# Kernel tuning notes

Hardware: AMD Instinct MI355X
Metric: run time of the kernel (lower is better)

The kernel has to match this reference:

```python
import jax, jax.numpy as jnp
import numpy as np

B, S, D, H, F = 4, 2048, 256, 8, 2  # batch, seq, input_size, heads, mlp factor
EPS = 1e-5


def _ln(x, g, b):
    m = jnp.mean(x, axis=-1, keepdims=True)
    v = jnp.var(x, axis=-1, keepdims=True)
    return (x - m) / jnp.sqrt(v + EPS) * g + b


def setup_inputs() -> dict:
    key = jax.random.key(0)
    ks = jax.random.split(key, 12)
    s = 1.0 / np.sqrt(D)
    return {
        "X":  jax.random.normal(ks[0], (B, S, D), jnp.float32),
        # Wide attention: each of H heads has full [D,D] Q/K/V projections (no bias)
        "Wq": jax.random.uniform(ks[1], (H, D, D), jnp.float32, -s, s),
        "Wk": jax.random.uniform(ks[2], (H, D, D), jnp.float32, -s, s),
        "Wv": jax.random.uniform(ks[3], (H, D, D), jnp.float32, -s, s),
        "Wz": jax.random.uniform(ks[4], (H * D, D), jnp.float32, -1.0 / np.sqrt(H * D), 1.0 / np.sqrt(H * D)),
        "bz": jnp.zeros((D,), jnp.float32),
        "W1": jax.random.uniform(ks[5], (D, F * D), jnp.float32, -s, s),
        "b1": jnp.zeros((F * D,), jnp.float32),
        "W2": jax.random.uniform(ks[6], (F * D, D), jnp.float32, -1.0 / np.sqrt(F * D), 1.0 / np.sqrt(F * D)),
        "b2": jnp.zeros((D,), jnp.float32),
        "g1": jnp.ones((D,), jnp.float32),
        "be1": jnp.zeros((D,), jnp.float32),
        "g2": jnp.ones((D,), jnp.float32),
        "be2": jnp.zeros((D,), jnp.float32),
    }


def reference(X, Wq, Wk, Wv, Wz, bz, W1, b1, W2, b2, g1, be1, g2, be2):
    scale = D ** (-0.25)  # applied to both q and k as in the source
    q = jnp.einsum('bsd,hde->hbse', X, Wq) * scale   # [H,B,S,D]
    k = jnp.einsum('btd,hde->hbte', X, Wk) * scale
    v = jnp.einsum('btd,hde->hbte', X, Wv)
    attn = jax.nn.softmax(jnp.einsum('hbse,hbte->hbst', q, k), axis=-1)  # [H,B,S,S]
    zh = jnp.einsum('hbst,hbte->hbse', attn, v)       # [H,B,S,D]
    # concat heads along feature dim (head order matters for Wz)
    zcat = jnp.transpose(zh, (1, 2, 0, 3)).reshape(B, S, H * D)
    z = zcat @ Wz + bz
    z = _ln(z + X, g1, be1)                            # dropout p=0 -> identity
    z_ff = jnp.maximum(z @ W1 + b1, 0.0) @ W2 + b2
    z = _ln(z_ff + z, g2, be2)
    attn_mean = jnp.mean(attn, axis=0)                 # [B,S,S]
    return z, attn_mean
```

## Files before the change

### kernel.cpp

```cpp
#include <hip/hip_runtime.h>
#include <cstdint>
#include <cstddef>

#define B_  4
#define S_  2048
#define D_  256
#define H_  8
#define FD_ 512
#define N_  (B_*S_)
#define HD_ (H_*D_)
#define EPS 1e-5f

typedef __attribute__((ext_vector_type(8))) short bf16x8;
typedef __attribute__((ext_vector_type(8))) unsigned short u16x8;
typedef __attribute__((ext_vector_type(4))) float f32x4;

__device__ __forceinline__ unsigned short f2bf(float f) {
  union { float f; unsigned u; } x; x.f = f;
  unsigned u = x.u;
  return (unsigned short)((u + 0x7FFFu + ((u >> 16) & 1u)) >> 16);
}
__device__ __forceinline__ float bf2f(unsigned short h) {
  union { unsigned u; float f; } x; x.u = ((unsigned)h) << 16; return x.f;
}

__device__ __forceinline__ void glds16(const void* gptr, void* ldsptr) {
  __builtin_amdgcn_global_load_lds(
      (__attribute__((address_space(1))) void*)gptr,
      (__attribute__((address_space(3))) void*)ldsptr,
      16, 0, 0);
}

__device__ __forceinline__ int sw32(int row, int u) {
  return (row*32 + ((u & 24) | ((u & 7) ^ (row & 7)))) * 8;
}
__device__ __forceinline__ int sw16(int row, int u) {
  return (row*16 + ((u & 8) | ((u & 7) ^ (row & 7)))) * 8;
}

__global__ __launch_bounds__(256) void cast_x_kernel(
    const float* __restrict__ X, unsigned short* __restrict__ Xb)
{
  const size_t i8 = ((size_t)blockIdx.x * 256 + threadIdx.x) * 8;
  float4 a = *(const float4*)&X[i8];
  float4 b = *(const float4*)&X[i8 + 4];
  u16x8 o;
  o[0]=f2bf(a.x); o[1]=f2bf(a.y); o[2]=f2bf(a.z); o[3]=f2bf(a.w);
  o[4]=f2bf(b.x); o[5]=f2bf(b.y); o[6]=f2bf(b.z); o[7]=f2bf(b.w);
  *(u16x8*)&Xb[i8] = o;
}

__global__ __launch_bounds__(256) void prep_w_kernel(
    const float* __restrict__ Wq, const float* __restrict__ Wk,
    const float* __restrict__ Wv, unsigned short* __restrict__ Wt)
{
  __shared__ float tile[64][65];
  const int tid = threadIdx.x;
  const int d0 = blockIdx.x * 64, e0 = blockIdx.y * 64;
  const int w = blockIdx.z;
  const float* src;
  float scale;
  if (w < 8)       { src = Wq + (size_t)w*D_*D_;      scale = 0.25f; }
  else if (w < 16) { src = Wk + (size_t)(w-8)*D_*D_;  scale = 0.25f; }
  else             { src = Wv + (size_t)(w-16)*D_*D_; scale = 1.0f;  }
  {
    int r = tid >> 2, c16 = (tid & 3) * 16;
    const float* s = src + (size_t)(d0 + r)*D_ + e0 + c16;
    #pragma unroll
    for (int u = 0; u < 4; ++u) *(float4*)&tile[r][c16 + u*4] = *(const float4*)(s + u*4);
  }
  __syncthreads();
  {
    int er = tid >> 2, dc = (tid & 3) * 16;
    u16x8 o0, o1;
    #pragma unroll
    for (int j = 0; j < 8; ++j) {
      o0[j] = f2bf(tile[dc + j][er] * scale);
      o1[j] = f2bf(tile[dc + 8 + j][er] * scale);
    }
    unsigned short* dst = Wt + ((size_t)w*D_ + e0 + er)*D_ + d0 + dc;
    *(u16x8*)(dst)     = o0;
    *(u16x8*)(dst + 8) = o1;
  }
}

__global__ __launch_bounds__(256) void tcast_kernel(
    const float* __restrict__ src, unsigned short* __restrict__ dst,
    int R, int C)
{
  __shared__ float tile[64][65];
  const int tid = threadIdx.x;
  const int r0 = blockIdx.x * 64, c0 = blockIdx.y * 64;
  {
    int r = tid >> 2, c16 = (tid & 3) * 16;
    const float* s = src + (size_t)(r0 + r)*C + c0 + c16;
    #pragma unroll
    for (int u = 0; u < 4; ++u) *(float4*)&tile[r][c16 + u*4] = *(const float4*)(s + u*4);
  }
  __syncthreads();
  {
    int cr = tid >> 2, rc = (tid & 3) * 16;
    u16x8 o0, o1;
    #pragma unroll
    for (int j = 0; j < 8; ++j) {
      o0[j] = f2bf(tile[rc + j][cr]);
      o1[j] = f2bf(tile[rc + 8 + j][cr]);
    }
    unsigned short* d = dst + (size_t)(c0 + cr)*R + r0 + rc;
    *(u16x8*)(d)     = o0;
    *(u16x8*)(d + 8) = o1;
  }
}

__global__ __launch_bounds__(256) void qkv_kernel(
    const unsigned short* __restrict__ Xb, const unsigned short* __restrict__ Wt,
    unsigned short* __restrict__ q, unsigned short* __restrict__ k,
    unsigned short* __restrict__ v)
{
  __shared__ unsigned short Xt[64*32*8];
  __shared__ unsigned short Wtile[64*32*8];
  const int tid = threadIdx.x;
  const int w4 = tid >> 6, lane = tid & 63;
  const int c = lane & 15, qd = lane >> 4;
  const int n0 = blockIdx.x * 64;
  const int e0 = blockIdx.y * 64;
  const int w  = blockIdx.z;

  unsigned short* obase;
  if (w < 8)       obase = q + (size_t)w*N_*D_;
  else if (w < 16) obase = k + (size_t)(w-8)*N_*D_;
  else             obase = v + (size_t)(w-16)*N_*D_;

  {
    const char* xg = (const char*)Xb + (size_t)n0*512;
    const char* wg = (const char*)Wt + ((size_t)w*D_ + e0)*512;
    #pragma unroll
    for (int i = 0; i < 8; ++i) {
      int g = w4*8 + i;
      int r = 2*g + (lane >> 5);
      int su = lane & 31;
      int u = (su & 24) | ((su & 7) ^ (r & 7));
      glds16(xg + (size_t)r*512 + u*16, &Xt[g*512]);
      glds16(wg + (size_t)r*512 + u*16, &Wtile[g*512]);
    }
  }
  __syncthreads();

  f32x4 sc[4];
  #pragma unroll
  for (int nc = 0; nc < 4; ++nc) sc[nc] = (f32x4){0.f,0.f,0.f,0.f};
  #pragma unroll
  for (int ks = 0; ks < 8; ++ks) {
    bf16x8 xa = *(const bf16x8*)&Xt[sw32(16*w4 + c, ks*4 + qd)];
    #pragma unroll
    for (int nc = 0; nc < 4; ++nc) {
      bf16x8 bf = *(const bf16x8*)&Wtile[sw32(nc*16 + c, ks*4 + qd)];
      sc[nc] = __builtin_amdgcn_mfma_f32_16x16x32_bf16(xa, bf, sc[nc], 0, 0, 0);
    }
  }
  #pragma unroll
  for (int nc = 0; nc < 4; ++nc)
    #pragma unroll
    for (int r = 0; r < 4; ++r)
      obase[(size_t)(n0 + 16*w4 + qd*4 + r)*D_ + e0 + nc*16 + c] = f2bf(sc[nc][r]);
}

__global__ __launch_bounds__(256) void vtrans_kernel(
    const unsigned short* __restrict__ vb, unsigned short* __restrict__ vT)
{
  __shared__ unsigned short tile[64][72];
  const int tid = threadIdx.x;
  const int t0 = blockIdx.x * 64, e0 = blockIdx.y * 64;
  const int h = blockIdx.z >> 2, b = blockIdx.z & 3;
  const size_t in_base = (size_t)h*N_*D_ + (size_t)b*S_*D_;
  {
    int r = tid >> 2, c16 = (tid & 3) * 16;
    const unsigned short* src = vb + in_base + (size_t)(t0 + r)*D_ + e0 + c16;
    *(u16x8*)&tile[r][c16]     = *(const u16x8*)(src);
    *(u16x8*)&tile[r][c16 + 8] = *(const u16x8*)(src + 8);
  }
  __syncthreads();
  {
    int er = tid >> 2, tt = (tid & 3) * 16;
    u16x8 o0, o1;
    #pragma unroll
    for (int j = 0; j < 8; ++j) { o0[j] = tile[tt+j][er]; o1[j] = tile[tt+8+j][er]; }
    unsigned short* dst = vT + ((size_t)(h*4 + b)*D_ + e0 + er)*S_ + t0 + tt;
    *(u16x8*)(dst)     = o0;
    *(u16x8*)(dst + 8) = o1;
  }
}

__global__ __launch_bounds__(256, 2) void attn_ol_kernel(
    const unsigned short* __restrict__ qb, const unsigned short* __restrict__ kb,
    const unsigned short* __restrict__ vT, unsigned short* __restrict__ zcatb,
    float* __restrict__ Lws)
{
  __shared__ unsigned short Kt[2][32*32*8];
  __shared__ unsigned short Vt[2][16*544];
  const int tid = threadIdx.x;
  const int w = tid >> 6, lane = tid & 63;
  const int c = lane & 15, qd = lane >> 4;
  const int wg = blockIdx.x;
  const int xcd = wg & 7;
  const int slot = wg >> 3;
  const int j = slot & 15;
  const int gg = slot >> 4;
  const int g = gg*8 + xcd;
  const int h = g >> 2, b = g & 3;
  const int s0 = j * 128;

  const size_t qkbase = (size_t)h*N_*D_ + (size_t)b*S_*D_;

  bf16x8 qa[2][8];
  #pragma unroll
  for (int mi = 0; mi < 2; ++mi) {
    const unsigned short* qrow = qb + qkbase + (size_t)(s0 + 32*w + 16*mi + c)*D_ + qd*8;
    #pragma unroll
    for (int ks = 0; ks < 8; ++ks) qa[mi][ks] = *(const bf16x8*)(qrow + ks*32);
  }

  f32x4 o[2][16];
  #pragma unroll
  for (int mi = 0; mi < 2; ++mi)
    #pragma unroll
    for (int i = 0; i < 16; ++i) o[mi][i] = (f32x4){0.f,0.f,0.f,0.f};
  float Lp[2] = {0.f, 0.f};

  const char* kB = (const char*)(kb + qkbase);
  const char* vB = (const char*)(vT + (size_t)(h*4 + b)*D_*S_);

  #define STAGE_OL(kt_, bi_)                                                   \
    {                                                                          \
      _Pragma("unroll")                                                        \
      for (int i = 0; i < 4; ++i) {                                            \
        int gq = w*4 + i;                                                      \
        int r = 2*gq + (lane >> 5);                                            \
        int Lg = ((r >> 2) & 3)*8 + (r >> 4)*4 + (r & 3);                      \
        int su = lane & 31;                                                    \
        int u = (su & 24) | ((su & 7) ^ (r & 7));                              \
        glds16(kB + ((size_t)(kt_)*32 + Lg)*512 + u*16, &Kt[bi_][gq*512]);     \
      }                                                                        \
      _Pragma("unroll")                                                        \
      for (int i = 0; i < 4; ++i) {                                            \
        int gq = w*4 + i;                                                      \
        int e = gq*16 + (lane >> 2);                                           \
        int qv = (lane & 3) ^ ((lane >> 3) & 3);                               \
        glds16(vB + (size_t)e*4096 + (size_t)(kt_)*64 + qv*16, &Vt[bi_][gq*544]);\
      }                                                                        \
    }

  STAGE_OL(0, 0);

  for (int kt = 0; kt < 64; ++kt) {
    const int bi = kt & 1;
    __syncthreads();
    if (kt + 1 < 64) STAGE_OL(kt + 1, bi ^ 1);

    f32x4 sc[2][2];
    #pragma unroll
    for (int mi = 0; mi < 2; ++mi)
      #pragma unroll
      for (int nc = 0; nc < 2; ++nc) sc[mi][nc] = (f32x4){0.f,0.f,0.f,0.f};
    #pragma unroll
    for (int ks = 0; ks < 8; ++ks) {
      bf16x8 kf0 = *(const bf16x8*)&Kt[bi][sw32(c,      ks*4 + qd)];
      bf16x8 kf1 = *(const bf16x8*)&Kt[bi][sw32(16 + c, ks*4 + qd)];
      #pragma unroll
      for (int mi = 0; mi < 2; ++mi) {
        sc[mi][0] = __builtin_amdgcn_mfma_f32_16x16x32_bf16(kf0, qa[mi][ks], sc[mi][0], 0, 0, 0);
        sc[mi][1] = __builtin_amdgcn_mfma_f32_16x16x32_bf16(kf1, qa[mi][ks], sc[mi][1], 0, 0, 0);
      }
    }
    bf16x8 pa[2];
    #pragma unroll
    for (int mi = 0; mi < 2; ++mi) {
      float ex[2][4];
      #pragma unroll
      for (int nc = 0; nc < 2; ++nc)
        #pragma unroll
        for (int r = 0; r < 4; ++r) {
          float p = __expf(sc[mi][nc][r]);
          ex[nc][r] = p;
          Lp[mi] += p;
        }
      union { unsigned u[4]; bf16x8 v; } cv;
      asm("v_cvt_pk_bf16_f32 %0, %1, %2" : "=v"(cv.u[0]) : "v"(ex[0][0]), "v"(ex[0][1]));
      asm("v_cvt_pk_bf16_f32 %0, %1, %2" : "=v"(cv.u[1]) : "v"(ex[0][2]), "v"(ex[0][3]));
      asm("v_cvt_pk_bf16_f32 %0, %1, %2" : "=v"(cv.u[2]) : "v"(ex[1][0]), "v"(ex[1][1]));
      asm("v_cvt_pk_bf16_f32 %0, %1, %2" : "=v"(cv.u[3]) : "v"(ex[1][2]), "v"(ex[1][3]));
      pa[mi] = cv.v;
    }
    #pragma unroll
    for (int ec = 0; ec < 16; ++ec) {
      bf16x8 vf = *(const bf16x8*)&Vt[bi][ec*544 + c*32 + (qd ^ ((c >> 1) & 3))*8];
      o[0][ec] = __builtin_amdgcn_mfma_f32_16x16x32_bf16(pa[0], vf, o[0][ec], 0, 0, 0);
      o[1][ec] = __builtin_amdgcn_mfma_f32_16x16x32_bf16(pa[1], vf, o[1][ec], 0, 0, 0);
    }
  }

  #pragma unroll
  for (int mi = 0; mi < 2; ++mi) {
    float L = Lp[mi];
    L += __shfl_xor(L, 16);
    L += __shfl_xor(L, 32);
    if (qd == 0)
      Lws[(size_t)h*N_ + b*S_ + s0 + 32*w + 16*mi + c] = L;
    float il[4];
    #pragma unroll
    for (int r = 0; r < 4; ++r)
      il[r] = 1.0f / __shfl(L, (lane & 48) | (qd*4 + r));
    #pragma unroll
    for (int ec = 0; ec < 16; ++ec)
      #pragma unroll
      for (int r = 0; r < 4; ++r)
        zcatb[(size_t)(b*S_ + s0 + 32*w + 16*mi + qd*4 + r)*HD_ + h*D_ + ec*16 + c] =
            f2bf(o[mi][ec][r] * il[r]);
  }
  #undef STAGE_OL
}

#define FATSMEM (73728 + 512)
__global__ __launch_bounds__(256, 2) void attn_mean_wz_kernel(
    const unsigned short* __restrict__ qb, const unsigned short* __restrict__ kb,
    const float* __restrict__ Lws, float* __restrict__ out_attn,
    const unsigned short* __restrict__ zcatb, const unsigned short* __restrict__ Wzt,
    const float* __restrict__ bz, const float* __restrict__ X,
    const float* __restrict__ g1, const float* __restrict__ be1,
    unsigned short* __restrict__ z1b)
{
  __shared__ __align__(16) char smem[FATSMEM];
  const int tid = threadIdx.x;
  const int w = tid >> 6, lane = tid & 63;
  const int c = lane & 15, qd = lane >> 4;
  const int bid = blockIdx.x;

  if (bid < 2048) {
    unsigned short (*Kt)[64*32*8] = (unsigned short (*)[64*32*8])smem;
    const int xcd = bid & 7;
    const int slot = bid >> 3;
    const int j = slot & 15;
    const int ggg = slot >> 4;
    const int g = ggg*8 + xcd;
    const int b = g >> 5;
    const int t0 = (g & 31) * 64;
    const int s0 = j * 128;

    float am[2][4][4] = {};

    #define STAGE_AM(h_, bi_)                                                  \
      {                                                                        \
        const char* kB = (const char*)(kb + (size_t)(h_)*N_*D_ + (size_t)b*S_*D_);\
        _Pragma("unroll")                                                      \
        for (int i = 0; i < 8; ++i) {                                          \
          int gq = w*8 + i;                                                    \
          int r = 2*gq + (lane >> 5);                                          \
          int su = lane & 31;                                                  \
          int u = (su & 24) | ((su & 7) ^ (r & 7));                            \
          glds16(kB + ((size_t)t0 + r)*512 + u*16, &Kt[bi_][gq*512]);          \
        }                                                                      \
      }

    STAGE_AM(0, 0);

    bf16x8 qa[2][8];
    #pragma unroll
    for (int mi = 0; mi < 2; ++mi) {
      const unsigned short* qrow = qb + (size_t)b*S_*D_ + (size_t)(s0 + 32*w + 16*mi + c)*D_ + qd*8;
      #pragma unroll
      for (int ks = 0; ks < 8; ++ks) qa[mi][ks] = *(const bf16x8*)(qrow + ks*32);
    }

    for (int h = 0; h < 8; ++h) {
      const int bi = h & 1;
      __syncthreads();
      if (h + 1 < 8) STAGE_AM(h + 1, bi ^ 1);

      float il[2][4];
      #pragma unroll
      for (int mi = 0; mi < 2; ++mi)
        #pragma unroll
        for (int r = 0; r < 4; ++r)
          il[mi][r] = 0.125f / Lws[(size_t)h*N_ + b*S_ + s0 + 32*w + 16*mi + qd*4 + r];

      bf16x8 qn[2][8];
      if (h + 1 < 8) {
        const size_t basen = (size_t)(h+1)*N_*D_ + (size_t)b*S_*D_;
        #pragma unroll
        for (int mi = 0; mi < 2; ++mi) {
          const unsigned short* qrow = qb + basen + (size_t)(s0 + 32*w + 16*mi + c)*D_ + qd*8;
          #pragma unroll
          for (int ks = 0; ks < 8; ++ks) qn[mi][ks] = *(const bf16x8*)(qrow + ks*32);
        }
      }

      f32x4 sc[2][4];
      #pragma unroll
      for (int mi = 0; mi < 2; ++mi)
        #pragma unroll
        for (int nc = 0; nc < 4; ++nc) sc[mi][nc] = (f32x4){0.f,0.f,0.f,0.f};
      #pragma unroll
      for (int ks = 0; ks < 8; ++ks) {
        #pragma unroll
        for (int nc = 0; nc < 4; ++nc) {
          bf16x8 kf = *(const bf16x8*)&Kt[bi][sw32(nc*16 + c, ks*4 + qd)];
          sc[0][nc] = __builtin_amdgcn_mfma_f32_16x16x32_bf16(qa[0][ks], kf, sc[0][nc], 0, 0, 0);
          sc[1][nc] = __builtin_amdgcn_mfma_f32_16x16x32_bf16(qa[1][ks], kf, sc[1][nc], 0, 0, 0);
        }
      }
      #pragma unroll
      for (int mi = 0; mi < 2; ++mi)
        #pragma unroll
        for (int nc = 0; nc < 4; ++nc)
          #pragma unroll
          for (int r = 0; r < 4; ++r)
            am[mi][nc][r] += __expf(sc[mi][nc][r]) * il[mi][r];

      if (h + 1 < 8) {
        #pragma unroll
        for (int mi = 0; mi < 2; ++mi)
          #pragma unroll
          for (int ks = 0; ks < 8; ++ks) qa[mi][ks] = qn[mi][ks];
      }
    }
    #pragma unroll
    for (int mi = 0; mi < 2; ++mi)
      #pragma unroll
      for (int nc = 0; nc < 4; ++nc)
        #pragma unroll
        for (int r = 0; r < 4; ++r)
          out_attn[(size_t)(b*S_ + s0 + 32*w + 16*mi + qd*4 + r)*S_ + t0 + nc*16 + c] =
              am[mi][nc][r];
    #undef STAGE_AM
  } else {
    unsigned short* At  = (unsigned short*)smem;
    unsigned short* Wt2 = (unsigned short*)(smem + 8192);
    float (*redS)[32] = (float (*)[32])(smem + 73728);
    float (*redQ)[32] = (float (*)[32])(smem + 73728 + 256);
    const int n0 = (bid - 2048) * 32;
    const int w4 = w;
    const int msub = w4 & 1, ehalf = w4 >> 1;

    f32x4 acc[8];
    #pragma unroll
    for (int nc = 0; nc < 8; ++nc) acc[nc] = (f32x4){0.f,0.f,0.f,0.f};

    for (int kc = 0; kc < 16; ++kc) {
      {
        const char* ab = (const char*)zcatb + (size_t)n0*4096 + (size_t)kc*256;
        #pragma unroll
        for (int i = 0; i < 2; ++i) {
          int g = w4*2 + i;
          int r = g*4 + (lane >> 4);
          int su = lane & 15;
          int u = (su & 8) | ((su & 7) ^ (r & 7));
          glds16(ab + (size_t)r*4096 + u*16, &At[g*512]);
        }
        const char* wb = (const char*)Wzt + (size_t)kc*256;
        #pragma unroll
        for (int i = 0; i < 16; ++i) {
          int g = w4*16 + i;
          int e = g*4 + (lane >> 4);
          int su = lane & 15;
          int u = (su & 8) | ((su & 7) ^ (e & 7));
          glds16(wb + (size_t)e*4096 + u*16, &Wt2[g*512]);
        }
      }
      __syncthreads();
      #pragma unroll
      for (int ks = 0; ks < 4; ++ks) {
        bf16x8 a = *(const bf16x8*)&At[sw16(msub*16 + c, ks*4 + qd)];
        #pragma unroll
        for (int nc = 0; nc < 8; ++nc) {
          bf16x8 bv = *(const bf16x8*)&Wt2[sw16(ehalf*128 + nc*16 + c, ks*4 + qd)];
          acc[nc] = __builtin_amdgcn_mfma_f32_16x16x32_bf16(a, bv, acc[nc], 0, 0, 0);
        }
      }
      __syncthreads();
    }

    float vals[8][4];
    float sum_[4] = {0.f,0.f,0.f,0.f}, sq_[4] = {0.f,0.f,0.f,0.f};
    #pragma unroll
    for (int nc = 0; nc < 8; ++nc) {
      int e = ehalf*128 + nc*16 + c;
      #pragma unroll
      for (int r = 0; r < 4; ++r) {
        int n = n0 + msub*16 + qd*4 + r;
        float v = acc[nc][r] + bz[e] + X[(size_t)n*D_ + e];
        vals[nc][r] = v;
        sum_[r] += v; sq_[r] += v*v;
      }
    }
    #pragma unroll
    for (int off = 1; off < 16; off <<= 1) {
      #pragma unroll
      for (int r = 0; r < 4; ++r) {
        sum_[r] += __shfl_xor(sum_[r], off);
        sq_[r]  += __shfl_xor(sq_[r],  off);
      }
    }
    if (c == 0) {
      #pragma unroll
      for (int r = 0; r < 4; ++r) {
        redS[ehalf][msub*16 + qd*4 + r] = sum_[r];
        redQ[ehalf][msub*16 + qd*4 + r] = sq_[r];
      }
    }
    __syncthreads();
    #pragma unroll
    for (int r = 0; r < 4; ++r) {
      int lr = msub*16 + qd*4 + r;
      float Sv = redS[0][lr] + redS[1][lr];
      float Qv = redQ[0][lr] + redQ[1][lr];
      float mean = Sv * (1.0f/D_);
      float var  = Qv * (1.0f/D_) - mean*mean;
      float rstd = rsqrtf(var + EPS);
      int n = n0 + lr;
      #pragma unroll
      for (int nc = 0; nc < 8; ++nc) {
        int e = ehalf*128 + nc*16 + c;
        z1b[(size_t)n*D_ + e] = f2bf((vals[nc][r] - mean)*rstd*g1[e] + be1[e]);
      }
    }
  }
}

__global__ __launch_bounds__(256) void mlp1_kernel(
    const unsigned short* __restrict__ z1b, const unsigned short* __restrict__ W1t,
    const float* __restrict__ b1, unsigned short* __restrict__ hbuf)
{
  __shared__ unsigned short At[64*32*8];
  __shared__ unsigned short Bt[64*32*8];
  const int tid = threadIdx.x;
  const int w4 = tid >> 6, lane = tid & 63;
  const int c = lane & 15, qd = lane >> 4;
  const int n0 = blockIdx.x * 64;
  const int f0 = blockIdx.y * 64;

  {
    const char* ag = (const char*)z1b + (size_t)n0*512;
    const char* bg = (const char*)W1t + (size_t)f0*512;
    #pragma unroll
    for (int i = 0; i < 8; ++i) {
      int g = w4*8 + i;
      int r = 2*g + (lane >> 5);
      int su = lane & 31;
      int u = (su & 24) | ((su & 7) ^ (r & 7));
      glds16(ag + (size_t)r*512 + u*16, &At[g*512]);
      glds16(bg + (size_t)r*512 + u*16, &Bt[g*512]);
    }
  }
  __syncthreads();

  f32x4 sc[4];
  #pragma unroll
  for (int nc = 0; nc < 4; ++nc) sc[nc] = (f32x4){0.f,0.f,0.f,0.f};
  #pragma unroll
  for (int ks = 0; ks < 8; ++ks) {
    bf16x8 xa = *(const bf16x8*)&At[sw32(16*w4 + c, ks*4 + qd)];
    #pragma unroll
    for (int nc = 0; nc < 4; ++nc) {
      bf16x8 bf = *(const bf16x8*)&Bt[sw32(nc*16 + c, ks*4 + qd)];
      sc[nc] = __builtin_amdgcn_mfma_f32_16x16x32_bf16(xa, bf, sc[nc], 0, 0, 0);
    }
  }
  #pragma unroll
  for (int nc = 0; nc < 4; ++nc) {
    int f = f0 + nc*16 + c;
    float bias = b1[f];
    #pragma unroll
    for (int r = 0; r < 4; ++r)
      hbuf[(size_t)(n0 + 16*w4 + qd*4 + r)*FD_ + f] = f2bf(fmaxf(sc[nc][r] + bias, 0.f));
  }
}

__global__ __launch_bounds__(256) void mlp2_kernel(
    const unsigned short* __restrict__ hbuf, const unsigned short* __restrict__ W2t,
    const float* __restrict__ b2, const unsigned short* __restrict__ z1b,
    const float* __restrict__ g2, const float* __restrict__ be2,
    float* __restrict__ out)
{
  __shared__ unsigned short At[32*16*8];
  __shared__ unsigned short Wt2[256*16*8];
  __shared__ float redS[2][32], redQ[2][32];
  const int tid = threadIdx.x;
  const int w4 = tid >> 6, lane = tid & 63;
  const int c = lane & 15, qd = lane >> 4;
  const int n0 = blockIdx.x * 32;
  const int msub = w4 & 1, ehalf = w4 >> 1;

  f32x4 acc[8];
  #pragma unroll
  for (int nc = 0; nc < 8; ++nc) acc[nc] = (f32x4){0.f,0.f,0.f,0.f};

  for (int kc = 0; kc < 4; ++kc) {
    {
      const char* ab = (const char*)hbuf + (size_t)n0*1024 + (size_t)kc*256;
      #pragma unroll
      for (int i = 0; i < 2; ++i) {
        int g = w4*2 + i;
        int r = g*4 + (lane >> 4);
        int su = lane & 15;
        int u = (su & 8) | ((su & 7) ^ (r & 7));
        glds16(ab + (size_t)r*1024 + u*16, &At[g*512]);
      }
      const char* wb = (const char*)W2t + (size_t)kc*256;
      #pragma unroll
      for (int i = 0; i < 16; ++i) {
        int g = w4*16 + i;
        int e = g*4 + (lane >> 4);
        int su = lane & 15;
        int u = (su & 8) | ((su & 7) ^ (e & 7));
        glds16(wb + (size_t)e*1024 + u*16, &Wt2[g*512]);
      }
    }
    __syncthreads();
    #pragma unroll
    for (int ks = 0; ks < 4; ++ks) {
      bf16x8 a = *(const bf16x8*)&At[sw16(msub*16 + c, ks*4 + qd)];
      #pragma unroll
      for (int nc = 0; nc < 8; ++nc) {
        bf16x8 bv = *(const bf16x8*)&Wt2[sw16(ehalf*128 + nc*16 + c, ks*4 + qd)];
        acc[nc] = __builtin_amdgcn_mfma_f32_16x16x32_bf16(a, bv, acc[nc], 0, 0, 0);
      }
    }
    __syncthreads();
  }

  float vals[8][4];
  float sum_[4] = {0.f,0.f,0.f,0.f}, sq_[4] = {0.f,0.f,0.f,0.f};
  #pragma unroll
  for (int nc = 0; nc < 8; ++nc) {
    int e = ehalf*128 + nc*16 + c;
    #pragma unroll
    for (int r = 0; r < 4; ++r) {
      int n = n0 + msub*16 + qd*4 + r;
      float v = acc[nc][r] + b2[e] + bf2f(z1b[(size_t)n*D_ + e]);
      vals[nc][r] = v;
      sum_[r] += v; sq_[r] += v*v;
    }
  }
  #pragma unroll
  for (int off = 1; off < 16; off <<= 1) {
    #pragma unroll
    for (int r = 0; r < 4; ++r) {
      sum_[r] += __shfl_xor(sum_[r], off);
      sq_[r]  += __shfl_xor(sq_[r],  off);
    }
  }
  if (c == 0) {
    #pragma unroll
    for (int r = 0; r < 4; ++r) {
      redS[ehalf][msub*16 + qd*4 + r] = sum_[r];
      redQ[ehalf][msub*16 + qd*4 + r] = sq_[r];
    }
  }
  __syncthreads();
  #pragma unroll
  for (int r = 0; r < 4; ++r) {
    int lr = msub*16 + qd*4 + r;
    float Sv = redS[0][lr] + redS[1][lr];
    float Qv = redQ[0][lr] + redQ[1][lr];
    float mean = Sv * (1.0f/D_);
    float var  = Qv * (1.0f/D_) - mean*mean;
    float rstd = rsqrtf(var + EPS);
    int n = n0 + lr;
    #pragma unroll
    for (int nc = 0; nc < 8; ++nc) {
      int e = ehalf*128 + nc*16 + c;
      out[(size_t)n*D_ + e] = (vals[nc][r] - mean)*rstd*g2[e] + be2[e];
    }
  }
}

extern "C" void kernel_launch(void* const* d_in, const int* in_sizes, int n_in,
                              void* d_out, int out_size, void* d_ws, size_t ws_size,
                              hipStream_t stream)
{
  (void)in_sizes; (void)n_in; (void)out_size; (void)ws_size;
  const float* X   = (const float*)d_in[0];
  const float* Wq  = (const float*)d_in[1];
  const float* Wk  = (const float*)d_in[2];
  const float* Wv  = (const float*)d_in[3];
  const float* Wz  = (const float*)d_in[4];
  const float* bz  = (const float*)d_in[5];
  const float* W1  = (const float*)d_in[6];
  const float* b1  = (const float*)d_in[7];
  const float* W2  = (const float*)d_in[8];
  const float* b2  = (const float*)d_in[9];
  const float* g1  = (const float*)d_in[10];
  const float* be1 = (const float*)d_in[11];
  const float* g2  = (const float*)d_in[12];
  const float* be2 = (const float*)d_in[13];

  char* p = (char*)d_ws;
  unsigned short* Xbb  = (unsigned short*)p; p += (size_t)N_*D_*2;
  unsigned short* Wtb  = (unsigned short*)p; p += (size_t)24*D_*D_*2;
  unsigned short* Wztb = (unsigned short*)p; p += (size_t)D_*HD_*2;
  unsigned short* W1tb = (unsigned short*)p; p += (size_t)FD_*D_*2;
  unsigned short* W2tb = (unsigned short*)p; p += (size_t)D_*FD_*2;
  unsigned short* qbuf = (unsigned short*)p; p += (size_t)H_*N_*D_*2;
  unsigned short* kbuf = (unsigned short*)p; p += (size_t)H_*N_*D_*2;
  unsigned short* vbuf = (unsigned short*)p; p += (size_t)H_*N_*D_*2;
  unsigned short* vTb  = (unsigned short*)p; p += (size_t)H_*N_*D_*2;
  float* Lws   = (float*)p; p += (size_t)H_*N_*4;
  unsigned short* zcatb = (unsigned short*)p; p += (size_t)N_*HD_*2;
  unsigned short* z1b   = (unsigned short*)p; p += (size_t)N_*D_*2;
  unsigned short* hbuf  = (unsigned short*)p;

  float* out_z    = (float*)d_out;
  float* out_attn = out_z + (size_t)N_*D_;

  cast_x_kernel<<<N_*D_/(256*8), 256, 0, stream>>>(X, Xbb);

  dim3 gW(4, 4, 24);
  prep_w_kernel<<<gW, 256, 0, stream>>>(Wq, Wk, Wv, Wtb);

  { dim3 g(HD_/64, D_/64);  tcast_kernel<<<g, 256, 0, stream>>>(Wz, Wztb, HD_, D_); }
  { dim3 g(D_/64, FD_/64);  tcast_kernel<<<g, 256, 0, stream>>>(W1, W1tb, D_, FD_); }
  { dim3 g(FD_/64, D_/64);  tcast_kernel<<<g, 256, 0, stream>>>(W2, W2tb, FD_, D_); }

  dim3 gA(N_/64, D_/64, 24);
  qkv_kernel<<<gA, 256, 0, stream>>>(Xbb, Wtb, qbuf, kbuf, vbuf);

  dim3 gT(S_/64, D_/64, H_*B_);
  vtrans_kernel<<<gT, 256, 0, stream>>>(vbuf, vTb);

  attn_ol_kernel<<<512, 256, 0, stream>>>(qbuf, kbuf, vTb, zcatb, Lws);

  attn_mean_wz_kernel<<<2304, 256, 0, stream>>>(
      qbuf, kbuf, Lws, out_attn, zcatb, Wztb, bz, X, g1, be1, z1b);

  dim3 gM1(N_/64, FD_/64);
  mlp1_kernel<<<gM1, 256, 0, stream>>>(z1b, W1tb, b1, hbuf);

  mlp2_kernel<<<N_/32, 256, 0, stream>>>(hbuf, W2tb, b2, z1b, g2, be2, out_z);
}
```

Measured before the change: 527.0 us.

## Merge prep kernels into one launch and fuse V transpose into QKV GEMM

Five preprocessing launches (X cast, QKV weight transpose/scale, and the Wz/W1/W2 transposes) become a single kernel that picks its task from the block index. The QKV projection kernel now writes V already transposed, staging the tile through the reused X shared buffer, so the separate vtrans kernel and the round trip of V through global memory are gone. This saves launch overhead and about 32 MB of memory traffic, at the cost of two extra barriers in the V-producing blocks and branchier prep code.

```diff
diff --git a/kernel.cpp b/kernel.cpp
--- a/kernel.cpp
+++ b/kernel.cpp
@@ -38,62 +38,68 @@
   return (row*16 + ((u & 8) | ((u & 7) ^ (row & 7)))) * 8;
 }
 
-__global__ __launch_bounds__(256) void cast_x_kernel(
-    const float* __restrict__ X, unsigned short* __restrict__ Xb)
-{
-  const size_t i8 = ((size_t)blockIdx.x * 256 + threadIdx.x) * 8;
-  float4 a = *(const float4*)&X[i8];
-  float4 b = *(const float4*)&X[i8 + 4];
-  u16x8 o;
-  o[0]=f2bf(a.x); o[1]=f2bf(a.y); o[2]=f2bf(a.z); o[3]=f2bf(a.w);
-  o[4]=f2bf(b.x); o[5]=f2bf(b.y); o[6]=f2bf(b.z); o[7]=f2bf(b.w);
-  *(u16x8*)&Xb[i8] = o;
-}
-
-__global__ __launch_bounds__(256) void prep_w_kernel(
+__global__ __launch_bounds__(256) void prep_fat_kernel(
+    const float* __restrict__ X, unsigned short* __restrict__ Xb,
     const float* __restrict__ Wq, const float* __restrict__ Wk,
-    const float* __restrict__ Wv, unsigned short* __restrict__ Wt)
+    const float* __restrict__ Wv, unsigned short* __restrict__ Wt,
+    const float* __restrict__ Wz, unsigned short* __restrict__ Wzt,
+    const float* __restrict__ W1, unsigned short* __restrict__ W1t,
+    const float* __restrict__ W2, unsigned short* __restrict__ W2t)
 {
   __shared__ float tile[64][65];
   const int tid = threadIdx.x;
-  const int d0 = blockIdx.x * 64, e0 = blockIdx.y * 64;
-  const int w = blockIdx.z;
+  const int bid = blockIdx.x;
+
+  if (bid < 1024) {
+    const size_t i8 = ((size_t)bid * 256 + tid) * 8;
+    float4 a = *(const float4*)&X[i8];
+    float4 b = *(const float4*)&X[i8 + 4];
+    u16x8 o;
+    o[0]=f2bf(a.x); o[1]=f2bf(a.y); o[2]=f2bf(a.z); o[3]=f2bf(a.w);
+    o[4]=f2bf(b.x); o[5]=f2bf(b.y); o[6]=f2bf(b.z); o[7]=f2bf(b.w);
+    *(u16x8*)&Xb[i8] = o;
+    return;
+  }
+
   const float* src;
-  float scale;
-  if (w < 8)       { src = Wq + (size_t)w*D_*D_;      scale = 0.25f; }
-  else if (w < 16) { src = Wk + (size_t)(w-8)*D_*D_;  scale = 0.25f; }
-  else             { src = Wv + (size_t)(w-16)*D_*D_; scale = 1.0f;  }
+  unsigned short* dst_base;
+  int R, C;
+  float scale = 1.0f;
+  int d0, e0;
+  bool is_prepw = false;
+  int wsel = 0;
+
+  if (bid < 1408) {
+    int idx = bid - 1024;
+    d0 = (idx & 3) * 64;
+    e0 = ((idx >> 2) & 3) * 64;
+    wsel = idx >> 4;
+    if (wsel < 8)       { src = Wq + (size_t)wsel*D_*D_;      scale = 0.25f; }
+    else if (wsel < 16) { src = Wk + (size_t)(wsel-8)*D_*D_;  scale = 0.25f; }
+    else                { src = Wv + (size_t)(wsel-16)*D_*D_; scale = 1.0f;  }
+    R = D_; C = D_;
+    dst_base = Wt;
+    is_prepw = true;
+  } else if (bid < 1536) {
+    int idx = bid - 1408;
+    d0 = (idx & 31) * 64;
+    e0 = (idx >> 5) * 64;
+    src = Wz; dst_base = Wzt; R = HD_; C = D_;
+  } else if (bid < 1568) {
+    int idx = bid - 1536;
+    d0 = (idx & 3) * 64;
+    e0 = (idx >> 2) * 64;
+    src = W1; dst_base = W1t; R = D_; C = FD_;
+  } else {
+    int idx = bid - 1568;
+    d0 = (idx & 7) * 64;
+    e0 = (idx >> 3) * 64;
+    src = W2; dst_base = W2t; R = FD_; C = D_;
+  }
+
   {
     int r = tid >> 2, c16 = (tid & 3) * 16;
-    const float* s = src + (size_t)(d0 + r)*D_ + e0 + c16;
-    #pragma unroll
-    for (int u = 0; u < 4; ++u) *(float4*)&tile[r][c16 + u*4] = *(const float4*)(s + u*4);
-  }
-  __syncthreads();
-  {
-    int er = tid >> 2, dc = (tid & 3) * 16;
-    u16x8 o0, o1;
-    #pragma unroll
-    for (int j = 0; j < 8; ++j) {
-      o0[j] = f2bf(tile[dc + j][er] * scale);
-      o1[j] = f2bf(tile[dc + 8 + j][er] * scale);
-    }
-    unsigned short* dst = Wt + ((size_t)w*D_ + e0 + er)*D_ + d0 + dc;
-    *(u16x8*)(dst)     = o0;
-    *(u16x8*)(dst + 8) = o1;
-  }
-}
-
-__global__ __launch_bounds__(256) void tcast_kernel(
-    const float* __restrict__ src, unsigned short* __restrict__ dst,
-    int R, int C)
-{
-  __shared__ float tile[64][65];
-  const int tid = threadIdx.x;
-  const int r0 = blockIdx.x * 64, c0 = blockIdx.y * 64;
-  {
-    int r = tid >> 2, c16 = (tid & 3) * 16;
-    const float* s = src + (size_t)(r0 + r)*C + c0 + c16;
+    const float* s = src + (size_t)(d0 + r)*C + e0 + c16;
     #pragma unroll
     for (int u = 0; u < 4; ++u) *(float4*)&tile[r][c16 + u*4] = *(const float4*)(s + u*4);
   }
@@ -103,10 +109,14 @@
     u16x8 o0, o1;
     #pragma unroll
     for (int j = 0; j < 8; ++j) {
-      o0[j] = f2bf(tile[rc + j][cr]);
-      o1[j] = f2bf(tile[rc + 8 + j][cr]);
-    }
-    unsigned short* d = dst + (size_t)(c0 + cr)*R + r0 + rc;
+      o0[j] = f2bf(tile[rc + j][cr] * scale);
+      o1[j] = f2bf(tile[rc + 8 + j][cr] * scale);
+    }
+    unsigned short* d;
+    if (is_prepw)
+      d = dst_base + ((size_t)wsel*D_ + e0 + cr)*D_ + d0 + rc;
+    else
+      d = dst_base + (size_t)(e0 + cr)*R + d0 + rc;
     *(u16x8*)(d)     = o0;
     *(u16x8*)(d + 8) = o1;
   }
@@ -115,7 +125,7 @@
 __global__ __launch_bounds__(256) void qkv_kernel(
     const unsigned short* __restrict__ Xb, const unsigned short* __restrict__ Wt,
     unsigned short* __restrict__ q, unsigned short* __restrict__ k,
-    unsigned short* __restrict__ v)
+    unsigned short* __restrict__ vT)
 {
   __shared__ unsigned short Xt[64*32*8];
   __shared__ unsigned short Wtile[64*32*8];
@@ -126,11 +136,6 @@
   const int e0 = blockIdx.y * 64;
   const int w  = blockIdx.z;
 
-  unsigned short* obase;
-  if (w < 8)       obase = q + (size_t)w*N_*D_;
-  else if (w < 16) obase = k + (size_t)(w-8)*N_*D_;
-  else             obase = v + (size_t)(w-16)*N_*D_;
-
   {
     const char* xg = (const char*)Xb + (size_t)n0*512;
     const char* wg = (const char*)Wt + ((size_t)w*D_ + e0)*512;
@@ -158,36 +163,36 @@
       sc[nc] = __builtin_amdgcn_mfma_f32_16x16x32_bf16(xa, bf, sc[nc], 0, 0, 0);
     }
   }
-  #pragma unroll
-  for (int nc = 0; nc < 4; ++nc)
-    #pragma unroll
-    for (int r = 0; r < 4; ++r)
-      obase[(size_t)(n0 + 16*w4 + qd*4 + r)*D_ + e0 + nc*16 + c] = f2bf(sc[nc][r]);
-}
-
-__global__ __launch_bounds__(256) void vtrans_kernel(
-    const unsigned short* __restrict__ vb, unsigned short* __restrict__ vT)
-{
-  __shared__ unsigned short tile[64][72];
-  const int tid = threadIdx.x;
-  const int t0 = blockIdx.x * 64, e0 = blockIdx.y * 64;
-  const int h = blockIdx.z >> 2, b = blockIdx.z & 3;
-  const size_t in_base = (size_t)h*N_*D_ + (size_t)b*S_*D_;
-  {
-    int r = tid >> 2, c16 = (tid & 3) * 16;
-    const unsigned short* src = vb + in_base + (size_t)(t0 + r)*D_ + e0 + c16;
-    *(u16x8*)&tile[r][c16]     = *(const u16x8*)(src);
-    *(u16x8*)&tile[r][c16 + 8] = *(const u16x8*)(src + 8);
-  }
-  __syncthreads();
-  {
-    int er = tid >> 2, tt = (tid & 3) * 16;
-    u16x8 o0, o1;
-    #pragma unroll
-    for (int j = 0; j < 8; ++j) { o0[j] = tile[tt+j][er]; o1[j] = tile[tt+8+j][er]; }
-    unsigned short* dst = vT + ((size_t)(h*4 + b)*D_ + e0 + er)*S_ + t0 + tt;
-    *(u16x8*)(dst)     = o0;
-    *(u16x8*)(dst + 8) = o1;
+
+  if (w < 16) {
+    unsigned short* obase = (w < 8) ? (q + (size_t)w*N_*D_)
+                                    : (k + (size_t)(w-8)*N_*D_);
+    #pragma unroll
+    for (int nc = 0; nc < 4; ++nc)
+      #pragma unroll
+      for (int r = 0; r < 4; ++r)
+        obase[(size_t)(n0 + 16*w4 + qd*4 + r)*D_ + e0 + nc*16 + c] = f2bf(sc[nc][r]);
+  } else {
+    const int h = w - 16;
+    const int b = n0 >> 11;
+    const int t0 = n0 & (S_ - 1);
+    unsigned short (*tile)[72] = (unsigned short (*)[72])Xt;
+    __syncthreads();
+    #pragma unroll
+    for (int nc = 0; nc < 4; ++nc)
+      #pragma unroll
+      for (int r = 0; r < 4; ++r)
+        tile[16*w4 + qd*4 + r][nc*16 + c] = f2bf(sc[nc][r]);
+    __syncthreads();
+    {
+      int er = tid >> 2, tt = (tid & 3) * 16;
+      u16x8 o0, o1;
+      #pragma unroll
+      for (int j = 0; j < 8; ++j) { o0[j] = tile[tt+j][er]; o1[j] = tile[tt+8+j][er]; }
+      unsigned short* dst = vT + ((size_t)(h*4 + b)*D_ + e0 + er)*S_ + t0 + tt;
+      *(u16x8*)(dst)     = o0;
+      *(u16x8*)(dst + 8) = o1;
+    }
   }
 }
 
@@ -708,24 +713,16 @@
   unsigned short* zcatb = (unsigned short*)p; p += (size_t)N_*HD_*2;
   unsigned short* z1b   = (unsigned short*)p; p += (size_t)N_*D_*2;
   unsigned short* hbuf  = (unsigned short*)p;
+  (void)vbuf;
 
   float* out_z    = (float*)d_out;
   float* out_attn = out_z + (size_t)N_*D_;
 
-  cast_x_kernel<<<N_*D_/(256*8), 256, 0, stream>>>(X, Xbb);
-
-  dim3 gW(4, 4, 24);
-  prep_w_kernel<<<gW, 256, 0, stream>>>(Wq, Wk, Wv, Wtb);
-
-  { dim3 g(HD_/64, D_/64);  tcast_kernel<<<g, 256, 0, stream>>>(Wz, Wztb, HD_, D_); }
-  { dim3 g(D_/64, FD_/64);  tcast_kernel<<<g, 256, 0, stream>>>(W1, W1tb, D_, FD_); }
-  { dim3 g(FD_/64, D_/64);  tcast_kernel<<<g, 256, 0, stream>>>(W2, W2tb, FD_, D_); }
+  prep_fat_kernel<<<1600, 256, 0, stream>>>(
+      X, Xbb, Wq, Wk, Wv, Wtb, Wz, Wztb, W1, W1tb, W2, W2tb);
 
   dim3 gA(N_/64, D_/64, 24);
-  qkv_kernel<<<gA, 256, 0, stream>>>(Xbb, Wtb, qbuf, kbuf, vbuf);
-
-  dim3 gT(S_/64, D_/64, H_*B_);
-  vtrans_kernel<<<gT, 256, 0, stream>>>(vbuf, vTb);
+  qkv_kernel<<<gA, 256, 0, stream>>>(Xbb, Wtb, qbuf, kbuf, vTb);
 
   attn_ol_kernel<<<512, 256, 0, stream>>>(qbuf, kbuf, vTb, zcatb, Lws);
 
```

Result: faster. 498.6 us (-5.4%).
